# Kernel tuning notes

Measured on AMD Instinct MI355X. Metric: run time of the kernel, lower is better.

The kernel has to match this reference:

```python
import jax, jax.numpy as jnp
import numpy as np

B, C, R, E, H = 32, 64, 63, 256, 4
D = E // H  # head dim = 64


def setup_inputs() -> dict:
    key = jax.random.key(0)
    ks = jax.random.split(key, 8)
    s = 0.02
    return {
        "x": jax.random.normal(ks[0], (B, C, R, E), jnp.float32),
        "real_cols": jax.random.randint(ks[1], (B,), 0, C),
        "cls_token": jax.random.normal(ks[2], (E,), jnp.float32),
        "w_in": (jax.random.normal(ks[3], (3 * E, E), jnp.float32) * s),
        "b_in": jnp.zeros((3 * E,), jnp.float32),
        "w_out": (jax.random.normal(ks[4], (E, E), jnp.float32) * s),
        "b_out": jnp.zeros((E,), jnp.float32),
        "ln_g": jnp.ones((E,), jnp.float32),
        "ln_b": jnp.zeros((E,), jnp.float32),
        "w1": (jax.random.normal(ks[5], (E, E), jnp.float32) * s),
        "b1": jnp.zeros((E,), jnp.float32),
        "w2": (jax.random.normal(ks[6], (E, E), jnp.float32) * s),
        "b2": jnp.zeros((E,), jnp.float32),
    }


def reference(x, real_cols, cls_token, w_in, b_in, w_out, b_out, ln_g, ln_b, w1, b1, w2, b2):
    # x: (B, C, R, E); one fused batched MHA+LN+FFN over all (B, C) columns.
    Bq, Cq, Rq, Eq = x.shape
    S = Rq + 1
    cls = jnp.broadcast_to(cls_token, (Bq, Cq, 1, Eq))
    seq = jnp.concatenate([cls, x], axis=2)  # (B,C,S,E)

    # torch MultiheadAttention in-projection: x @ W^T + b, packed q|k|v
    qkv = seq @ w_in.T + b_in  # (B,C,S,3E)
    q, k, v = jnp.split(qkv, 3, axis=-1)
    q = q.reshape(Bq, Cq, S, H, D)
    k = k.reshape(Bq, Cq, S, H, D)
    v = v.reshape(Bq, Cq, S, H, D)

    scale = 1.0 / jnp.sqrt(jnp.asarray(D, x.dtype))
    scores = jnp.einsum('bcqhd,bckhd->bchqk', q, k) * scale  # (B,C,H,S,S)
    attn = jax.nn.softmax(scores, axis=-1)
    ctx = jnp.einsum('bchqk,bckhd->bcqhd', attn, v).reshape(Bq, Cq, S, Eq)
    attn_out = ctx @ w_out.T + b_out  # (B,C,S,E)

    # LayerNorm (biased variance, eps=1e-5 as in torch)
    mu = attn_out.mean(axis=-1, keepdims=True)
    var = ((attn_out - mu) ** 2).mean(axis=-1, keepdims=True)
    ln = (attn_out - mu) / jnp.sqrt(var + 1e-5) * ln_g + ln_b

    ffn = jax.nn.relu(ln @ w1.T + b1) @ w2.T + b2
    out = ln + ffn  # (B,C,S,E)

    rep = out[:, :, 0, :]  # rep_mode == 'cls'

    # columns >= real_cols[b] are zero-padded, matching the original loop
    mask = jnp.arange(Cq)[None, :] < real_cols[:, None]
    return jnp.where(mask[..., None], rep, jnp.zeros((), x.dtype))
```

## Files before the change

### kernel.cpp

```cpp
#include <hip/hip_runtime.h>
#include <hip/hip_bf16.h>
#include <cstdint>

typedef unsigned short u16;
typedef uint32_t u32;

#define Bq 32
#define Cq 64
#define Rq 63
#define NB 4

__device__ __forceinline__ float bflo(u32 u){ return __uint_as_float(u << 16); }
__device__ __forceinline__ float bfhi(u32 u){ return __uint_as_float(u & 0xffff0000u); }
__device__ __forceinline__ float bf1(u16 u){ return __uint_as_float(((u32)u) << 16); }
__device__ __forceinline__ u16 tobf(float f){ __hip_bfloat16 h = __float2bfloat16(f); return *(u16*)&h; }

__device__ __forceinline__ bool dtype_is_bf16(const void* ln_g){
    return *(const u32*)ln_g == 0x3F803F80u;
}
__device__ __forceinline__ float ldin(const void* p, int i, bool bf){
    return bf ? bf1(((const u16*)p)[i]) : ((const float*)p)[i];
}


__global__ __launch_bounds__(256) void prep_kernel(
    const void* __restrict__ cls, const void* __restrict__ w_in,
    const void* __restrict__ b_in, const void* __restrict__ w_out,
    const void* __restrict__ w1, const void* __restrict__ w2,
    const void* __restrict__ ln_g_flag,
    float* __restrict__ uf, float* __restrict__ sbf,
    u16* __restrict__ wvT, u16* __restrict__ woT,
    u16* __restrict__ w1T, u16* __restrict__ w2T)
{
    const bool bf = dtype_is_bf16(ln_g_flag);
    const int tid = threadIdx.x;
    const int blk = blockIdx.x;
    __shared__ float q0[256];
    __shared__ float clsf[256];

    if (blk < 256) {
        const int e = blk, j = tid;
        const int dsti = ((j >> 3) * 256 + e) * 8 + (j & 7);
        wvT[dsti] = tobf(ldin(w_in, (512 + e) * 256 + j, bf));
        woT[dsti] = tobf(ldin(w_out, e * 256 + j, bf));
        w1T[dsti] = tobf(ldin(w1,    e * 256 + j, bf));
        w2T[dsti] = tobf(ldin(w2,    e * 256 + j, bf));
        return;
    }

    const int h = blk - 256;
    clsf[tid] = ldin(cls, tid, bf);
    __syncthreads();

    {
        float acc = ldin(b_in, tid, bf);
        #pragma unroll 8
        for (int j = 0; j < 256; ++j)
            acc += ldin(w_in, tid * 256 + j, bf) * clsf[j];
        q0[tid] = acc;
    }
    __syncthreads();

    {
        float ua = 0.f;
        #pragma unroll 8
        for (int d = 0; d < 64; ++d)
            ua += q0[h * 64 + d] * ldin(w_in, (256 + h * 64 + d) * 256 + tid, bf);
        uf[h * 256 + tid] = ua * 0.125f;
    }
    if (tid < 64) {
        float p = q0[h * 64 + tid] * ldin(b_in, 256 + h * 64 + tid, bf);
        #pragma unroll
        for (int off = 32; off; off >>= 1) p += __shfl_xor(p, off);
        if (tid == 0) sbf[h] = p * 0.125f;
    }
}

__global__ __launch_bounds__(256) void attn_kernel(
    const void* __restrict__ x, const int* __restrict__ real_cols,
    const void* __restrict__ cls, const void* __restrict__ ln_g,
    const float* __restrict__ uf, const float* __restrict__ sbf,
    u16* __restrict__ sbuf)
{
    const bool bf = dtype_is_bf16(ln_g);
    const int tid = threadIdx.x;
    const int bc = blockIdx.x;
    const int b = bc >> 6, c = bc & 63;
    if (c >= real_cols[b]) return;

    __shared__ __align__(16) u16   lds_seq[64 * 260];
    __shared__ __align__(16) float lds_u[1024];
    __shared__ __align__(16) float lds_a[256];
    __shared__ float lds_sb[4];

    #pragma unroll
    for (int q = 0; q < 4; ++q) lds_u[q * 256 + tid] = uf[q * 256 + tid];
    if (tid < 4) lds_sb[tid] = sbf[tid];

    if (bf) {
        const u16* xr = (const u16*)x + (size_t)bc * (Rq * 256);
        #pragma unroll
        for (int k = 0; k < 8; ++k) {
            int idx = k * 256 + tid;
            if (idx < 2016) {
                uint4 val = *(const uint4*)(xr + idx * 8);
                int tt = (idx >> 5) + 1;
                int col = (idx & 31) * 8;
                uint2* p = (uint2*)&lds_seq[tt * 260 + col];
                p[0] = make_uint2(val.x, val.y);
                p[1] = make_uint2(val.z, val.w);
            }
        }
        if (tid < 32) {
            uint4 val = *(const uint4*)((const u16*)cls + tid * 8);
            uint2* p = (uint2*)&lds_seq[tid * 8];
            p[0] = make_uint2(val.x, val.y);
            p[1] = make_uint2(val.z, val.w);
        }
    } else {
        const float* xr = (const float*)x + (size_t)bc * (Rq * 256);
        #pragma unroll
        for (int k = 0; k < 16; ++k) {
            int idx = k * 256 + tid;
            if (idx < 4032) {
                float4 v = *(const float4*)(xr + idx * 4);
                int tt = (idx >> 6) + 1;
                int col = (idx & 63) * 4;
                u32 lo = ((u32)tobf(v.y) << 16) | tobf(v.x);
                u32 hi = ((u32)tobf(v.w) << 16) | tobf(v.z);
                *(uint2*)&lds_seq[tt * 260 + col] = make_uint2(lo, hi);
            }
        }
        if (tid < 64) {
            float4 v = *(const float4*)((const float*)cls + tid * 4);
            u32 lo = ((u32)tobf(v.y) << 16) | tobf(v.x);
            u32 hi = ((u32)tobf(v.w) << 16) | tobf(v.z);
            *(uint2*)&lds_seq[tid * 4] = make_uint2(lo, hi);
        }
    }
    __syncthreads();

    const int h = tid >> 6, t = tid & 63;
    float sc = lds_sb[h];
    {
        const u16* srow = &lds_seq[t * 260];
        const float* uh = &lds_u[h * 256];
        #pragma unroll 8
        for (int j = 0; j < 256; j += 4) {
            uint2 pv = *(const uint2*)&srow[j];
            float4 uv = *(const float4*)&uh[j];
            sc += bflo(pv.x) * uv.x + bfhi(pv.x) * uv.y
                + bflo(pv.y) * uv.z + bfhi(pv.y) * uv.w;
        }
    }
    float m = sc;
    #pragma unroll
    for (int off = 32; off; off >>= 1) m = fmaxf(m, __shfl_xor(m, off));
    float ev = __expf(sc - m);
    float sum = ev;
    #pragma unroll
    for (int off = 32; off; off >>= 1) sum += __shfl_xor(sum, off);
    lds_a[t * 4 + h] = ev / sum;
    __syncthreads();

    {
        float s0 = 0.f, s1 = 0.f, s2 = 0.f, s3 = 0.f;
        #pragma unroll 4
        for (int tt = 0; tt < 64; ++tt) {
            float v = bf1(lds_seq[tt * 260 + tid]);
            float4 at = *(const float4*)&lds_a[tt * 4];
            s0 += at.x * v; s1 += at.y * v; s2 += at.z * v; s3 += at.w * v;
        }
        u16* sp = sbuf + (size_t)bc * 1024;
        sp[tid]       = tobf(s0);
        sp[256 + tid] = tobf(s1);
        sp[512 + tid] = tobf(s2);
        sp[768 + tid] = tobf(s3);
    }
}

template<int NBv>
__device__ __forceinline__ void dotN(const u16* __restrict__ wp,
                                     const float* __restrict__ vecs, int vstride,
                                     float* __restrict__ acc)
{
    #pragma unroll 2
    for (int j8 = 0; j8 < 32; ++j8) {
        uint4 w = *(const uint4*)(wp + j8 * 2048);
        float w0 = bflo(w.x), w1_ = bfhi(w.x), w2_ = bflo(w.y), w3 = bfhi(w.y);
        float w4 = bflo(w.z), w5 = bfhi(w.z), w6 = bflo(w.w), w7 = bfhi(w.w);
        #pragma unroll
        for (int i = 0; i < NBv; ++i) {
            const float* v = vecs + i * vstride + j8 * 8;
            float4 a = *(const float4*)v;
            float4 bq = *(const float4*)(v + 4);
            acc[i] += w0 * a.x + w1_ * a.y + w2_ * a.z + w3 * a.w
                    + w4 * bq.x + w5 * bq.y + w6 * bq.z + w7 * bq.w;
        }
    }
}

__global__ __launch_bounds__(256) void ffn_kernel(
    const int* __restrict__ real_cols,
    const void* __restrict__ b_in, const void* __restrict__ b_out,
    const void* __restrict__ ln_g, const void* __restrict__ ln_b,
    const void* __restrict__ b1p, const void* __restrict__ b2p,
    const u16* __restrict__ sbuf,
    const u16* __restrict__ wvT, const u16* __restrict__ woT,
    const u16* __restrict__ w1T, const u16* __restrict__ w2T,
    void* __restrict__ out)
{
    const bool bf = dtype_is_bf16(ln_g);
    const int tid = threadIdx.x;
    const int b = blockIdx.x >> 4;
    const int g = blockIdx.x & 15;
    const int c0 = g * NB;
    const int rc = real_cols[b];
    const int e = tid;

    if (c0 >= rc) {
        #pragma unroll
        for (int i = 0; i < NB; ++i) {
            size_t oi = (((size_t)b << 6) + c0 + i) * 256 + e;
            if (bf) ((u16*)out)[oi] = 0; else ((float*)out)[oi] = 0.f;
        }
        return;
    }

    __shared__ __align__(16) float lds_s[NB * 1024];
    __shared__ __align__(16) float lds_ctx[NB * 256];
    __shared__ __align__(16) float lds_ln[NB * 256];
    __shared__ __align__(16) float lds_h1[NB * 256];
    __shared__ float lds_redA[4 * NB];
    __shared__ float lds_redB[4 * NB];

    #pragma unroll
    for (int i = 0; i < NB; ++i) {
        int c = c0 + i;
        if (c < rc) {
            const u32* sp = (const u32*)(sbuf + ((((size_t)b << 6) + c) << 10));
            u32 a0 = sp[tid], a1 = sp[tid + 256];
            lds_s[i * 1024 + 2 * tid]       = bflo(a0);
            lds_s[i * 1024 + 2 * tid + 1]   = bfhi(a0);
            lds_s[i * 1024 + 512 + 2 * tid]     = bflo(a1);
            lds_s[i * 1024 + 512 + 2 * tid + 1] = bfhi(a1);
        } else {
            lds_s[i * 1024 + 2 * tid] = 0.f;   lds_s[i * 1024 + 2 * tid + 1] = 0.f;
            lds_s[i * 1024 + 512 + 2 * tid] = 0.f; lds_s[i * 1024 + 512 + 2 * tid + 1] = 0.f;
        }
    }
    __syncthreads();

    const int h = tid >> 6;

    {
        float acc[NB];
        float bv = ldin(b_in, 512 + e, bf);
        #pragma unroll
        for (int i = 0; i < NB; ++i) acc[i] = bv;
        dotN<NB>(wvT + e * 8, &lds_s[h * 256], 1024, acc);
        #pragma unroll
        for (int i = 0; i < NB; ++i) lds_ctx[i * 256 + e] = acc[i];
    }
    __syncthreads();

    float ao[NB];
    {
        float bo = ldin(b_out, e, bf);
        #pragma unroll
        for (int i = 0; i < NB; ++i) ao[i] = bo;
        dotN<NB>(woT + e * 8, lds_ctx, 256, ao);
    }

    const int lane = tid & 63, wv = tid >> 6;
    float mu[NB];
    {
        float r[NB];
        #pragma unroll
        for (int i = 0; i < NB; ++i) r[i] = ao[i];
        #pragma unroll
        for (int off = 32; off; off >>= 1) {
            #pragma unroll
            for (int i = 0; i < NB; ++i) r[i] += __shfl_xor(r[i], off);
        }
        if (lane == 0) {
            #pragma unroll
            for (int i = 0; i < NB; ++i) lds_redA[wv * NB + i] = r[i];
        }
    }
    __syncthreads();
    #pragma unroll
    for (int i = 0; i < NB; ++i)
        mu[i] = (lds_redA[i] + lds_redA[NB + i] + lds_redA[2 * NB + i] + lds_redA[3 * NB + i]) * (1.f / 256.f);

    float lnv[NB];
    {
        float r[NB];
        #pragma unroll
        for (int i = 0; i < NB; ++i) { float d = ao[i] - mu[i]; r[i] = d * d; }
        #pragma unroll
        for (int off = 32; off; off >>= 1) {
            #pragma unroll
            for (int i = 0; i < NB; ++i) r[i] += __shfl_xor(r[i], off);
        }
        if (lane == 0) {
            #pragma unroll
            for (int i = 0; i < NB; ++i) lds_redB[wv * NB + i] = r[i];
        }
    }
    __syncthreads();
    {
        float gg = ldin(ln_g, e, bf), bb = ldin(ln_b, e, bf);
        #pragma unroll
        for (int i = 0; i < NB; ++i) {
            float var = (lds_redB[i] + lds_redB[NB + i] + lds_redB[2 * NB + i] + lds_redB[3 * NB + i]) * (1.f / 256.f);
            lnv[i] = (ao[i] - mu[i]) * rsqrtf(var + 1e-5f) * gg + bb;
            lds_ln[i * 256 + e] = lnv[i];
        }
    }
    __syncthreads();

    {
        float h1[NB];
        float bv = ldin(b1p, e, bf);
        #pragma unroll
        for (int i = 0; i < NB; ++i) h1[i] = bv;
        dotN<NB>(w1T + e * 8, lds_ln, 256, h1);
        #pragma unroll
        for (int i = 0; i < NB; ++i) lds_h1[i * 256 + e] = fmaxf(h1[i], 0.f);
    }
    __syncthreads();

    {
        float o[NB];
        float bv = ldin(b2p, e, bf);
        #pragma unroll
        for (int i = 0; i < NB; ++i) o[i] = lnv[i] + bv;
        dotN<NB>(w2T + e * 8, lds_h1, 256, o);
        #pragma unroll
        for (int i = 0; i < NB; ++i) {
            int c = c0 + i;
            float val = (c < rc) ? o[i] : 0.f;
            size_t oi = (((size_t)b << 6) + c) * 256 + e;
            if (bf) ((u16*)out)[oi] = tobf(val); else ((float*)out)[oi] = val;
        }
    }
}

extern "C" void kernel_launch(void* const* d_in, const int* in_sizes, int n_in,
                              void* d_out, int out_size, void* d_ws, size_t ws_size,
                              hipStream_t stream) {
    const void* x     = d_in[0];
    const int* rcols  = (const int*)d_in[1];
    const void* cls   = d_in[2];
    const void* w_in  = d_in[3];
    const void* b_in  = d_in[4];
    const void* w_out = d_in[5];
    const void* b_out = d_in[6];
    const void* ln_g  = d_in[7];
    const void* ln_b  = d_in[8];
    const void* w1    = d_in[9];
    const void* b1    = d_in[10];
    const void* w2    = d_in[11];
    const void* b2    = d_in[12];

    char* ws = (char*)d_ws;
    float* uf  = (float*)(ws);
    float* sbf = (float*)(ws + 4096);
    u16* wvT = (u16*)(ws + 4608);
    u16* woT = (u16*)(ws + 4608 + 131072);
    u16* w1T = (u16*)(ws + 4608 + 2 * 131072);
    u16* w2T = (u16*)(ws + 4608 + 3 * 131072);
    u16* sbuf = (u16*)(ws + 528896);

    prep_kernel<<<260, 256, 0, stream>>>(cls, w_in, b_in, w_out, w1, w2, ln_g,
                                         uf, sbf, wvT, woT, w1T, w2T);
    attn_kernel<<<Bq * Cq, 256, 0, stream>>>(x, rcols, cls, ln_g, uf, sbf, sbuf);
    ffn_kernel<<<Bq * (Cq / NB), 256, 0, stream>>>(rcols, b_in, b_out, ln_g, ln_b,
                                                   b1, b2, sbuf,
                                                   wvT, woT, w1T, w2T, d_out);
}
```

Measured before the change: 281.6 us.

## Fuse attention into FFN kernel and vectorize prep cls projection

```diff
diff --git a/kernel.cpp b/kernel.cpp
--- a/kernel.cpp
+++ b/kernel.cpp
@@ -36,7 +36,7 @@
     const int tid = threadIdx.x;
     const int blk = blockIdx.x;
     __shared__ float q0[256];
-    __shared__ float clsf[256];
+    __shared__ __align__(16) float clsf[256];
 
     if (blk < 256) {
         const int e = blk, j = tid;
@@ -54,9 +54,26 @@
 
     {
         float acc = ldin(b_in, tid, bf);
-        #pragma unroll 8
-        for (int j = 0; j < 256; ++j)
-            acc += ldin(w_in, tid * 256 + j, bf) * clsf[j];
+        if (bf) {
+            const u16* wr = (const u16*)w_in + tid * 256;
+            #pragma unroll 8
+            for (int j8 = 0; j8 < 32; ++j8) {
+                uint4 w = *(const uint4*)(wr + j8 * 8);
+                const float* c = &clsf[j8 * 8];
+                acc += bflo(w.x) * c[0] + bfhi(w.x) * c[1]
+                     + bflo(w.y) * c[2] + bfhi(w.y) * c[3]
+                     + bflo(w.z) * c[4] + bfhi(w.z) * c[5]
+                     + bflo(w.w) * c[6] + bfhi(w.w) * c[7];
+            }
+        } else {
+            const float4* wr = (const float4*)((const float*)w_in + tid * 256);
+            #pragma unroll 8
+            for (int j4 = 0; j4 < 64; ++j4) {
+                float4 w = wr[j4];
+                float4 c = *(const float4*)&clsf[j4 * 4];
+                acc += w.x * c.x + w.y * c.y + w.z * c.z + w.w * c.w;
+            }
+        }
         q0[tid] = acc;
     }
     __syncthreads();
@@ -73,109 +90,6 @@
         #pragma unroll
         for (int off = 32; off; off >>= 1) p += __shfl_xor(p, off);
         if (tid == 0) sbf[h] = p * 0.125f;
-    }
-}
-
-__global__ __launch_bounds__(256) void attn_kernel(
-    const void* __restrict__ x, const int* __restrict__ real_cols,
-    const void* __restrict__ cls, const void* __restrict__ ln_g,
-    const float* __restrict__ uf, const float* __restrict__ sbf,
-    u16* __restrict__ sbuf)
-{
-    const bool bf = dtype_is_bf16(ln_g);
-    const int tid = threadIdx.x;
-    const int bc = blockIdx.x;
-    const int b = bc >> 6, c = bc & 63;
-    if (c >= real_cols[b]) return;
-
-    __shared__ __align__(16) u16   lds_seq[64 * 260];
-    __shared__ __align__(16) float lds_u[1024];
-    __shared__ __align__(16) float lds_a[256];
-    __shared__ float lds_sb[4];
-
-    #pragma unroll
-    for (int q = 0; q < 4; ++q) lds_u[q * 256 + tid] = uf[q * 256 + tid];
-    if (tid < 4) lds_sb[tid] = sbf[tid];
-
-    if (bf) {
-        const u16* xr = (const u16*)x + (size_t)bc * (Rq * 256);
-        #pragma unroll
-        for (int k = 0; k < 8; ++k) {
-            int idx = k * 256 + tid;
-            if (idx < 2016) {
-                uint4 val = *(const uint4*)(xr + idx * 8);
-                int tt = (idx >> 5) + 1;
-                int col = (idx & 31) * 8;
-                uint2* p = (uint2*)&lds_seq[tt * 260 + col];
-                p[0] = make_uint2(val.x, val.y);
-                p[1] = make_uint2(val.z, val.w);
-            }
-        }
-        if (tid < 32) {
-            uint4 val = *(const uint4*)((const u16*)cls + tid * 8);
-            uint2* p = (uint2*)&lds_seq[tid * 8];
-            p[0] = make_uint2(val.x, val.y);
-            p[1] = make_uint2(val.z, val.w);
-        }
-    } else {
-        const float* xr = (const float*)x + (size_t)bc * (Rq * 256);
-        #pragma unroll
-        for (int k = 0; k < 16; ++k) {
-            int idx = k * 256 + tid;
-            if (idx < 4032) {
-                float4 v = *(const float4*)(xr + idx * 4);
-                int tt = (idx >> 6) + 1;
-                int col = (idx & 63) * 4;
-                u32 lo = ((u32)tobf(v.y) << 16) | tobf(v.x);
-                u32 hi = ((u32)tobf(v.w) << 16) | tobf(v.z);
-                *(uint2*)&lds_seq[tt * 260 + col] = make_uint2(lo, hi);
-            }
-        }
-        if (tid < 64) {
-            float4 v = *(const float4*)((const float*)cls + tid * 4);
-            u32 lo = ((u32)tobf(v.y) << 16) | tobf(v.x);
-            u32 hi = ((u32)tobf(v.w) << 16) | tobf(v.z);
-            *(uint2*)&lds_seq[tid * 4] = make_uint2(lo, hi);
-        }
-    }
-    __syncthreads();
-
-    const int h = tid >> 6, t = tid & 63;
-    float sc = lds_sb[h];
-    {
-        const u16* srow = &lds_seq[t * 260];
-        const float* uh = &lds_u[h * 256];
-        #pragma unroll 8
-        for (int j = 0; j < 256; j += 4) {
-            uint2 pv = *(const uint2*)&srow[j];
-            float4 uv = *(const float4*)&uh[j];
-            sc += bflo(pv.x) * uv.x + bfhi(pv.x) * uv.y
-                + bflo(pv.y) * uv.z + bfhi(pv.y) * uv.w;
-        }
-    }
-    float m = sc;
-    #pragma unroll
-    for (int off = 32; off; off >>= 1) m = fmaxf(m, __shfl_xor(m, off));
-    float ev = __expf(sc - m);
-    float sum = ev;
-    #pragma unroll
-    for (int off = 32; off; off >>= 1) sum += __shfl_xor(sum, off);
-    lds_a[t * 4 + h] = ev / sum;
-    __syncthreads();
-
-    {
-        float s0 = 0.f, s1 = 0.f, s2 = 0.f, s3 = 0.f;
-        #pragma unroll 4
-        for (int tt = 0; tt < 64; ++tt) {
-            float v = bf1(lds_seq[tt * 260 + tid]);
-            float4 at = *(const float4*)&lds_a[tt * 4];
-            s0 += at.x * v; s1 += at.y * v; s2 += at.z * v; s3 += at.w * v;
-        }
-        u16* sp = sbuf + (size_t)bc * 1024;
-        sp[tid]       = tobf(s0);
-        sp[256 + tid] = tobf(s1);
-        sp[512 + tid] = tobf(s2);
-        sp[768 + tid] = tobf(s3);
     }
 }
 
@@ -200,12 +114,13 @@
     }
 }
 
-__global__ __launch_bounds__(256) void ffn_kernel(
-    const int* __restrict__ real_cols,
+__global__ __launch_bounds__(256) void fused_kernel(
+    const void* __restrict__ x, const int* __restrict__ real_cols,
+    const void* __restrict__ cls,
     const void* __restrict__ b_in, const void* __restrict__ b_out,
     const void* __restrict__ ln_g, const void* __restrict__ ln_b,
     const void* __restrict__ b1p, const void* __restrict__ b2p,
-    const u16* __restrict__ sbuf,
+    const float* __restrict__ uf, const float* __restrict__ sbf,
     const u16* __restrict__ wvT, const u16* __restrict__ woT,
     const u16* __restrict__ w1T, const u16* __restrict__ w2T,
     void* __restrict__ out)
@@ -227,6 +142,10 @@
         return;
     }
 
+    __shared__ __align__(16) u16   lds_seq[64 * 260];
+    __shared__ __align__(16) float lds_u[1024];
+    __shared__ __align__(16) float lds_a[256];
+    __shared__ float lds_sb[4];
     __shared__ __align__(16) float lds_s[NB * 1024];
     __shared__ __align__(16) float lds_ctx[NB * 256];
     __shared__ __align__(16) float lds_ln[NB * 256];
@@ -235,21 +154,110 @@
     __shared__ float lds_redB[4 * NB];
 
     #pragma unroll
+    for (int q = 0; q < 4; ++q) lds_u[q * 256 + tid] = uf[q * 256 + tid];
+    if (tid < 4) lds_sb[tid] = sbf[tid];
+
+    if (bf) {
+        if (tid < 32) {
+            uint4 val = *(const uint4*)((const u16*)cls + tid * 8);
+            uint2* p = (uint2*)&lds_seq[tid * 8];
+            p[0] = make_uint2(val.x, val.y);
+            p[1] = make_uint2(val.z, val.w);
+        }
+    } else {
+        if (tid < 64) {
+            float4 v = *(const float4*)((const float*)cls + tid * 4);
+            u32 lo = ((u32)tobf(v.y) << 16) | tobf(v.x);
+            u32 hi = ((u32)tobf(v.w) << 16) | tobf(v.z);
+            *(uint2*)&lds_seq[tid * 4] = make_uint2(lo, hi);
+        }
+    }
+
+    const int hw = tid >> 6, lt = tid & 63;
+
     for (int i = 0; i < NB; ++i) {
-        int c = c0 + i;
-        if (c < rc) {
-            const u32* sp = (const u32*)(sbuf + ((((size_t)b << 6) + c) << 10));
-            u32 a0 = sp[tid], a1 = sp[tid + 256];
-            lds_s[i * 1024 + 2 * tid]       = bflo(a0);
-            lds_s[i * 1024 + 2 * tid + 1]   = bfhi(a0);
-            lds_s[i * 1024 + 512 + 2 * tid]     = bflo(a1);
-            lds_s[i * 1024 + 512 + 2 * tid + 1] = bfhi(a1);
-        } else {
-            lds_s[i * 1024 + 2 * tid] = 0.f;   lds_s[i * 1024 + 2 * tid + 1] = 0.f;
-            lds_s[i * 1024 + 512 + 2 * tid] = 0.f; lds_s[i * 1024 + 512 + 2 * tid + 1] = 0.f;
-        }
-    }
-    __syncthreads();
+        const int c = c0 + i;
+        const int bc = (b << 6) + c;
+        const bool act = (c < rc);
+
+        if (act) {
+            if (bf) {
+                const u16* xr = (const u16*)x + (size_t)bc * (Rq * 256);
+                #pragma unroll
+                for (int k = 0; k < 8; ++k) {
+                    int idx = k * 256 + tid;
+                    if (idx < 2016) {
+                        uint4 val = *(const uint4*)(xr + idx * 8);
+                        int tt = (idx >> 5) + 1;
+                        int col = (idx & 31) * 8;
+                        uint2* p = (uint2*)&lds_seq[tt * 260 + col];
+                        p[0] = make_uint2(val.x, val.y);
+                        p[1] = make_uint2(val.z, val.w);
+                    }
+                }
+            } else {
+                const float* xr = (const float*)x + (size_t)bc * (Rq * 256);
+                #pragma unroll
+                for (int k = 0; k < 16; ++k) {
+                    int idx = k * 256 + tid;
+                    if (idx < 4032) {
+                        float4 v = *(const float4*)(xr + idx * 4);
+                        int tt = (idx >> 6) + 1;
+                        int col = (idx & 63) * 4;
+                        u32 lo = ((u32)tobf(v.y) << 16) | tobf(v.x);
+                        u32 hi = ((u32)tobf(v.w) << 16) | tobf(v.z);
+                        *(uint2*)&lds_seq[tt * 260 + col] = make_uint2(lo, hi);
+                    }
+                }
+            }
+        }
+        __syncthreads();
+
+        if (act) {
+            float sc = lds_sb[hw];
+            {
+                const u16* srow = &lds_seq[lt * 260];
+                const float* uh = &lds_u[hw * 256];
+                #pragma unroll 8
+                for (int j = 0; j < 256; j += 4) {
+                    uint2 pv = *(const uint2*)&srow[j];
+                    float4 uv = *(const float4*)&uh[j];
+                    sc += bflo(pv.x) * uv.x + bfhi(pv.x) * uv.y
+                        + bflo(pv.y) * uv.z + bfhi(pv.y) * uv.w;
+                }
+            }
+            float m = sc;
+            #pragma unroll
+            for (int off = 32; off; off >>= 1) m = fmaxf(m, __shfl_xor(m, off));
+            float ev = __expf(sc - m);
+            float sum = ev;
+            #pragma unroll
+            for (int off = 32; off; off >>= 1) sum += __shfl_xor(sum, off);
+            lds_a[lt * 4 + hw] = ev / sum;
+        }
+        __syncthreads();
+
+        {
+            float* sp = &lds_s[i * 1024];
+            if (act) {
+                float s0 = 0.f, s1 = 0.f, s2 = 0.f, s3 = 0.f;
+                #pragma unroll 4
+                for (int tt = 0; tt < 64; ++tt) {
+                    float v = bf1(lds_seq[tt * 260 + tid]);
+                    float4 at = *(const float4*)&lds_a[tt * 4];
+                    s0 += at.x * v; s1 += at.y * v; s2 += at.z * v; s3 += at.w * v;
+                }
+                sp[tid]       = s0;
+                sp[256 + tid] = s1;
+                sp[512 + tid] = s2;
+                sp[768 + tid] = s3;
+            } else {
+                sp[tid] = 0.f; sp[256 + tid] = 0.f;
+                sp[512 + tid] = 0.f; sp[768 + tid] = 0.f;
+            }
+        }
+        __syncthreads();
+    }
 
     const int h = tid >> 6;
 
@@ -371,12 +379,11 @@
     u16* woT = (u16*)(ws + 4608 + 131072);
     u16* w1T = (u16*)(ws + 4608 + 2 * 131072);
     u16* w2T = (u16*)(ws + 4608 + 3 * 131072);
-    u16* sbuf = (u16*)(ws + 528896);
 
     prep_kernel<<<260, 256, 0, stream>>>(cls, w_in, b_in, w_out, w1, w2, ln_g,
                                          uf, sbf, wvT, woT, w1T, w2T);
-    attn_kernel<<<Bq * Cq, 256, 0, stream>>>(x, rcols, cls, ln_g, uf, sbf, sbuf);
-    ffn_kernel<<<Bq * (Cq / NB), 256, 0, stream>>>(rcols, b_in, b_out, ln_g, ln_b,
-                                                   b1, b2, sbuf,
-                                                   wvT, woT, w1T, w2T, d_out);
-}
+    fused_kernel<<<Bq * (Cq / NB), 256, 0, stream>>>(x, rcols, cls,
+                                                     b_in, b_out, ln_g, ln_b,
+                                                     b1, b2, uf, sbf,
+                                                     wvT, woT, w1T, w2T, d_out);
+}
```

New measurement: 260.2 us. 1.08x faster.
